# Optimization experiments

Measured on AMD Instinct MI355X. Metric: run time of the kernel, lower is better.

## Reference

```python
import jax, jax.numpy as jnp
import numpy as np

D = 512          # hidden_dim
H_HEADS = 8
DH = D // H_HEADS  # 64
L = 6            # n_layers
P = 8            # patch size
KT = 3           # temporal kernel
Z_DIM = 32
FILM_SCALE = 0.5
ROPE_BASE = 10000.0
EPS = 1e-5


def layer_norm(x, g, b):
    mu = x.mean(-1, keepdims=True)
    var = ((x - mu) ** 2).mean(-1, keepdims=True)
    return (x - mu) * jax.lax.rsqrt(var + EPS) * g + b


def rotate_half(x):
    x1, x2 = jnp.split(x, 2, axis=-1)
    return jnp.concatenate([-x2, x1], axis=-1)


def rope_time(T, dtype):
    half = DH // 2
    inv_freq = ROPE_BASE ** (-(jnp.arange(half, dtype=dtype) / half))  # (half,)
    angles = jnp.arange(T, dtype=dtype)[:, None] * inv_freq[None, :]   # (T, half)
    sin = jnp.concatenate([jnp.sin(angles), jnp.sin(angles)], -1)      # (T, DH)
    cos = jnp.concatenate([jnp.cos(angles), jnp.cos(angles)], -1)
    return sin, cos


def setup_inputs() -> dict:
    key = jax.random.key(0)
    ks = iter(jax.random.split(key, 64))
    n = lambda shape, s=0.02: jax.random.normal(next(ks), shape, jnp.float32) * s
    inp = {
        "x": jax.random.normal(next(ks), (16, 32, 3, 64, 64), jnp.float32),
        "z": jax.random.normal(next(ks), (16, 32, Z_DIM), jnp.float32),
        # tokenizer: CausalConv3d (kt,ph,pw)=(3,8,8), stride (1,8,8)
        "conv_w": n((D, 3, KT, P, P)),
        "conv_b": jnp.zeros((D,), jnp.float32),
        "tok_g": jnp.ones((D,), jnp.float32),
        "tok_b": jnp.zeros((D,), jnp.float32),
        # FiLM from z -> (gamma, beta)
        "film_w": n((Z_DIM, 2 * D)),
        "film_b": jnp.zeros((2 * D,), jnp.float32),
        # transformer blocks (stacked over L)
        "ln1_g": jnp.ones((L, D), jnp.float32), "ln1_b": jnp.zeros((L, D), jnp.float32),
        "kqv_w": n((L, D, 3 * D)), "kqv_b": jnp.zeros((L, 3 * D), jnp.float32),
        "proj_w": n((L, D, D)), "proj_b": jnp.zeros((L, D), jnp.float32),
        "ln2_g": jnp.ones((L, D), jnp.float32), "ln2_b": jnp.zeros((L, D), jnp.float32),
        "mlp_w1": n((L, D, 4 * D)), "mlp_b1": jnp.zeros((L, 4 * D), jnp.float32),
        "mlp_w2": n((L, 4 * D, D)), "mlp_b2": jnp.zeros((L, D), jnp.float32),
        "rs_attn": jnp.full((L,), 0.5, jnp.float32),
        "rs_mlp": jnp.full((L,), 0.5, jnp.float32),
        # scoring head
        "head_g": jnp.ones((D,), jnp.float32), "head_b": jnp.zeros((D,), jnp.float32),
        "head_w": n((D, 1)), "head_bias": jnp.zeros((1,), jnp.float32),
    }
    return inp


def _forward(x, z, conv_w, conv_b, tok_g, tok_b, film_w, film_b,
             ln1_g, ln1_b, kqv_w, kqv_b, proj_w, proj_b, ln2_g, ln2_b,
             mlp_w1, mlp_b1, mlp_w2, mlp_b2, rs_attn, rs_mlp,
             head_g, head_b, head_w, head_bias):
    B, T, C, Himg, Wimg = x.shape
    # ---- SpatialTemporalTokenizer: causal Conv3d (pad time on past only) ----
    xc = jnp.transpose(x, (0, 2, 1, 3, 4))  # [B,C,T,H,W]
    y = jax.lax.conv_general_dilated(
        xc, conv_w, window_strides=(1, P, P),
        padding=[(KT - 1, 0), (0, 0), (0, 0)],
        dimension_numbers=("NCDHW", "OIDHW", "NCDHW"))
    y = y + conv_b[None, :, None, None, None]          # [B,D,T,Hn,Wn]
    Hn, Wn = y.shape[3], y.shape[4]
    tok = jnp.transpose(y, (0, 2, 3, 4, 1)).reshape(B, T, Hn * Wn, D)
    tok = layer_norm(tok, tok_g, tok_b)                 # [B,T,N,D]
    # ---- FiLM conditioning from z ----
    gb = z @ film_w + film_b                            # [B,T,2D]
    gamma, beta = jnp.split(gb, 2, axis=-1)
    tok = (1.0 + FILM_SCALE * gamma)[:, :, None, :] * tok + (FILM_SCALE * beta)[:, :, None, :]
    # ---- spatial pooling -> temporal sequence ----
    h = tok.mean(axis=2)                                # [B,T,D]
    # ---- transformer stack (causal, time RoPE, pre-LN, gated residuals) ----
    sin_t, cos_t = rope_time(T, h.dtype)                # (T, DH)
    causal = jnp.tril(jnp.ones((T, T), bool))
    neg_inf = jnp.finfo(h.dtype).min
    for i in range(L):
        xi = layer_norm(h, ln1_g[i], ln1_b[i])
        kqv = xi @ kqv_w[i] + kqv_b[i]                  # [B,T,3D]
        k, q, v = jnp.split(kqv, 3, axis=-1)            # torch chunk order: k,q,v
        sh = lambda t: t.reshape(B, T, H_HEADS, DH).transpose(0, 2, 1, 3)  # [B,h,T,d]
        q, k, v = sh(q), sh(k), sh(v)
        q = q * cos_t + rotate_half(q) * sin_t
        k = k * cos_t + rotate_half(k) * sin_t
        att = jnp.einsum("bhqd,bhkd->bhqk", q, k) / np.sqrt(DH)
        att = jnp.where(causal[None, None], att, neg_inf)
        att = jax.nn.softmax(att, axis=-1)
        yv = jnp.einsum("bhqk,bhkd->bhqd", att, v)
        yv = yv.transpose(0, 2, 1, 3).reshape(B, T, D)
        attn_out = yv @ proj_w[i] + proj_b[i]
        h = h + rs_attn[i] * attn_out
        x2 = layer_norm(h, ln2_g[i], ln2_b[i])
        m = jax.nn.gelu(x2 @ mlp_w1[i] + mlp_b1[i], approximate=False) @ mlp_w2[i] + mlp_b2[i]
        h = h + rs_mlp[i] * m
    # ---- per-timestep score head ----
    h = layer_norm(h, head_g, head_b)
    score = (h @ head_w + head_bias)[..., 0]            # [B,T]
    return score


def reference(x, z, conv_w, conv_b, tok_g, tok_b, film_w, film_b,
              ln1_g, ln1_b, kqv_w, kqv_b, proj_w, proj_b, ln2_g, ln2_b,
              mlp_w1, mlp_b1, mlp_w2, mlp_b2, rs_attn, rs_mlp,
              head_g, head_b, head_w, head_bias):
    return _forward(x, z, conv_w, conv_b, tok_g, tok_b, film_w, film_b,
                    ln1_g, ln1_b, kqv_w, kqv_b, proj_w, proj_b, ln2_g, ln2_b,
                    mlp_w1, mlp_b1, mlp_w2, mlp_b2, rs_attn, rs_mlp,
                    head_g, head_b, head_w, head_bias)
```

## Files before the change

kernel.cpp:

```cpp
#include <hip/hip_runtime.h>
#include <math.h>

#define EPS 1e-5f

typedef __attribute__((ext_vector_type(8))) short short8;
typedef __attribute__((ext_vector_type(4))) float f32x4;

__device__ __forceinline__ short f2bf(float f) {
    unsigned u = __float_as_uint(f);
    u += 0x7fffu + ((u >> 16) & 1u);
    return (short)(u >> 16);
}
__device__ __forceinline__ float bf2f(short s) {
    return __uint_as_float(((unsigned)(unsigned short)s) << 16);
}
__device__ __forceinline__ void async16(const void* g, void* l) {
    __builtin_amdgcn_global_load_lds(
        (const __attribute__((address_space(1))) unsigned*)g,
        (__attribute__((address_space(3))) unsigned*)l, 16, 0, 0);
}

__device__ __forceinline__ float block_reduce_sum_256(float v, float* red) {
    #pragma unroll
    for (int o = 32; o > 0; o >>= 1) v += __shfl_down(v, o, 64);
    __syncthreads();
    if ((threadIdx.x & 63) == 0) red[threadIdx.x >> 6] = v;
    __syncthreads();
    return red[0] + red[1] + red[2] + red[3];
}

__global__ __launch_bounds__(256) void film_kernel(
    const float* __restrict__ z, const float* __restrict__ fw,
    const float* __restrict__ fb, float* __restrict__ gb) {
    int bt = blockIdx.x;
    __shared__ float zs[32];
    if (threadIdx.x < 32) zs[threadIdx.x] = z[bt * 32 + threadIdx.x];
    __syncthreads();
    for (int j = threadIdx.x; j < 1024; j += 256) {
        float acc = fb[j];
        #pragma unroll
        for (int k = 0; k < 32; k++) acc = fmaf(zs[k], fw[k * 1024 + j], acc);
        gb[bt * 1024 + j] = acc;
    }
}

__global__ __launch_bounds__(256) void cvt_kernel(
    const float* __restrict__ src, short* __restrict__ dst, int n) {
    int i = blockIdx.x * 256 + threadIdx.x;
    if (i < n) dst[i] = f2bf(src[i]);
}

__global__ __launch_bounds__(256) void xcast_kernel(
    const float* __restrict__ x, short* __restrict__ xbf, int n8) {
    int i = blockIdx.x * 256 + threadIdx.x;
    if (i < n8) {
        float4 a = *(const float4*)(x + (size_t)i * 8);
        float4 b = *(const float4*)(x + (size_t)i * 8 + 4);
        short8 o = {f2bf(a.x), f2bf(a.y), f2bf(a.z), f2bf(a.w),
                    f2bf(b.x), f2bf(b.y), f2bf(b.z), f2bf(b.w)};
        *(short8*)(xbf + (size_t)i * 8) = o;
    }
}

__global__ __launch_bounds__(256) void tcast_kernel(
    const float* __restrict__ src, short* __restrict__ dst, int K, int N) {
    __shared__ float tile[32][33];
    src += (size_t)blockIdx.z * K * N;
    dst += (size_t)blockIdx.z * N * K;
    int n0 = blockIdx.x * 32, k0 = blockIdx.y * 32;
    int lx = threadIdx.x & 31, ly = threadIdx.x >> 5;
    #pragma unroll
    for (int i = 0; i < 32; i += 8)
        tile[ly + i][lx] = src[(size_t)(k0 + ly + i) * N + n0 + lx];
    __syncthreads();
    #pragma unroll
    for (int i = 0; i < 32; i += 8)
        dst[(size_t)(n0 + ly + i) * K + k0 + lx] = f2bf(tile[lx][ly + i]);
}

__global__ __launch_bounds__(256) void conv_gemm(
    const short* __restrict__ xbf, const short* __restrict__ wbf,
    const float* __restrict__ cb, short* __restrict__ tok) {
    __shared__ short As[128 * 64];
    __shared__ short Bs[128 * 64];
    int tid = threadIdx.x;
    int n0 = blockIdx.x * 128, m0 = blockIdx.y * 128;
    int wave = tid >> 6, lane = tid & 63, quad = lane >> 4, l16 = lane & 15;
    int wm = wave & 1, wn = wave >> 1;

    int segA[4], tA[4];
    long long base0[4];
    #pragma unroll
    for (int e = 0; e < 4; e++) {
        int p = e * 256 + tid;
        int row = p >> 3;
        segA[e] = (p & 7) ^ (row & 7);
        int m = m0 + row;
        int bt = m >> 6, nn = m & 63;
        int b = bt >> 5, t = bt & 31;
        int hn = nn >> 3, wn2 = nn & 7;
        tA[e] = t;
        base0[e] = (((long long)(b * 32 + t - 2) * 3) << 12)
                   + (long long)(hn * 8) * 64 + wn2 * 8;
    }

    f32x4 acc[4][4];
    #pragma unroll
    for (int mt = 0; mt < 4; mt++)
        #pragma unroll
        for (int nt = 0; nt < 4; nt++) acc[mt][nt] = (f32x4){0.f, 0.f, 0.f, 0.f};

    for (int k0 = 0; k0 < 576; k0 += 64) {
        #pragma unroll
        for (int e = 0; e < 4; e++) {
            int p = e * 256 + tid;
            int n = p >> 3, seg = (p & 7) ^ (n & 7);
            async16(wbf + (size_t)(n0 + n) * 576 + k0 + seg * 8, Bs + p * 8);
        }
        #pragma unroll
        for (int e = 0; e < 4; e++) {
            int p = e * 256 + tid;
            int ks = (k0 >> 3) + segA[e];
            int ch = (ks >= 24) + (ks >= 48);
            int r = ks - ch * 24;
            int kt = r >> 3, ph = r & 7;
            short8 v8 = (short8){0, 0, 0, 0, 0, 0, 0, 0};
            if (tA[e] + kt >= 2)
                v8 = *(const short8*)(xbf + base0[e]
                        + ((long long)(kt * 3 + ch) << 12) + ph * 64);
            *(short8*)(As + p * 8) = v8;
        }
        __syncthreads();
        #pragma unroll
        for (int ksub = 0; ksub < 2; ksub++) {
            int ccb = ksub * 4 + quad;
            short8 af[4], bf[4];
            #pragma unroll
            for (int mt = 0; mt < 4; mt++) {
                int row = wm * 64 + mt * 16 + l16;
                af[mt] = *(const short8*)(As + (row * 8 + (ccb ^ (row & 7))) * 8);
            }
            #pragma unroll
            for (int nt = 0; nt < 4; nt++) {
                int row = wn * 64 + nt * 16 + l16;
                bf[nt] = *(const short8*)(Bs + (row * 8 + (ccb ^ (row & 7))) * 8);
            }
            #pragma unroll
            for (int mt = 0; mt < 4; mt++)
                #pragma unroll
                for (int nt = 0; nt < 4; nt++)
                    acc[mt][nt] = __builtin_amdgcn_mfma_f32_16x16x32_bf16(
                        af[mt], bf[nt], acc[mt][nt], 0, 0, 0);
        }
        __syncthreads();
    }
    #pragma unroll
    for (int mt = 0; mt < 4; mt++)
        #pragma unroll
        for (int nt = 0; nt < 4; nt++)
            #pragma unroll
            for (int reg = 0; reg < 4; reg++) {
                int m = m0 + wm * 64 + mt * 16 + quad * 4 + reg;
                int n = n0 + wn * 64 + nt * 16 + l16;
                tok[(size_t)m * 512 + n] = f2bf(acc[mt][nt][reg] + cb[n]);
            }
}

__global__ __launch_bounds__(256) void tok_post(
    const short* __restrict__ tok, const float* __restrict__ tg,
    const float* __restrict__ tb, const float* __restrict__ gb,
    float* __restrict__ h) {
    __shared__ float mu_s[64], inv_s[64];
    __shared__ float red[4][512];
    int bt = blockIdx.x, tid = threadIdx.x;
    int wave = tid >> 6, lane = tid & 63;
    {
        int tokn = wave * 16 + (lane >> 2), part = lane & 3;
        const short* p = tok + (size_t)(bt * 64 + tokn) * 512 + part * 128;
        float s = 0.f, ss = 0.f;
        #pragma unroll
        for (int i = 0; i < 16; i++) {
            short8 v = *(const short8*)(p + i * 8);
            #pragma unroll
            for (int j = 0; j < 8; j++) {
                float f = bf2f(v[j]);
                s += f; ss += f * f;
            }
        }
        s += __shfl_xor(s, 1, 64); ss += __shfl_xor(ss, 1, 64);
        s += __shfl_xor(s, 2, 64); ss += __shfl_xor(ss, 2, 64);
        if (part == 0) {
            float mu = s * (1.f / 512.f);
            float var = ss * (1.f / 512.f) - mu * mu;
            mu_s[tokn] = mu;
            inv_s[tokn] = rsqrtf(var + EPS);
        }
    }
    __syncthreads();
    float hacc[8] = {0.f, 0.f, 0.f, 0.f, 0.f, 0.f, 0.f, 0.f};
    int c0 = lane * 8;
    for (int it = 0; it < 16; it++) {
        int n = it * 4 + wave;
        float mu = mu_s[n], inv = inv_s[n];
        short8 v = *(const short8*)(tok + (size_t)(bt * 64 + n) * 512 + c0);
        #pragma unroll
        for (int j = 0; j < 8; j++) hacc[j] += (bf2f(v[j]) - mu) * inv;
    }
    #pragma unroll
    for (int j = 0; j < 8; j++) red[wave][c0 + j] = hacc[j];
    __syncthreads();
    #pragma unroll
    for (int cc = 0; cc < 2; cc++) {
        int c = tid + cc * 256;
        float S = red[0][c] + red[1][c] + red[2][c] + red[3][c];
        float G  = 1.f + 0.5f * gb[bt * 1024 + c];
        float Be = 0.5f * gb[bt * 1024 + 512 + c];
        h[bt * 512 + c] = G * (tg[c] * (S * (1.f / 64.f)) + tb[c]) + Be;
    }
}

__global__ __launch_bounds__(256) void gemm_ln(
    const float* __restrict__ hsrc, const float* __restrict__ lng,
    const float* __restrict__ lnb, const short* __restrict__ Bw,
    const float* __restrict__ bias, int N, int mode,
    float* __restrict__ outf, short* __restrict__ outb) {
    __shared__ short As[32 * 512];
    __shared__ short Bs[128 * 128];
    __shared__ float mu_s[32], inv_s[32];
    int tid = threadIdx.x;
    int m0 = blockIdx.y * 32, n0 = blockIdx.x * 128;
    {
        int row = tid >> 3, l8 = tid & 7;
        const float* hp = hsrc + (size_t)(m0 + row) * 512 + l8 * 64;
        float s = 0.f, ss = 0.f;
        #pragma unroll
        for (int i = 0; i < 16; i++) {
            float4 v = *(const float4*)(hp + i * 4);
            s += v.x + v.y + v.z + v.w;
            ss += v.x * v.x + v.y * v.y + v.z * v.z + v.w * v.w;
        }
        s += __shfl_xor(s, 1, 64); ss += __shfl_xor(ss, 1, 64);
        s += __shfl_xor(s, 2, 64); ss += __shfl_xor(ss, 2, 64);
        s += __shfl_xor(s, 4, 64); ss += __shfl_xor(ss, 4, 64);
        if (l8 == 0) {
            float mu = s * (1.f / 512.f);
            float var = ss * (1.f / 512.f) - mu * mu;
            mu_s[row] = mu;
            inv_s[row] = rsqrtf(var + EPS);
        }
    }
    __syncthreads();
    #pragma unroll
    for (int e = 0; e < 8; e++) {
        int lc = e * 256 + tid;
        int row = lc >> 6, cc = lc & 63;
        float mu = mu_s[row], inv = inv_s[row];
        const float* hp = hsrc + (size_t)(m0 + row) * 512 + cc * 8;
        float4 a = *(const float4*)hp, b = *(const float4*)(hp + 4);
        float4 g0 = *(const float4*)(lng + cc * 8), g1 = *(const float4*)(lng + cc * 8 + 4);
        float4 b0 = *(const float4*)(lnb + cc * 8), b1 = *(const float4*)(lnb + cc * 8 + 4);
        short8 o = {f2bf((a.x - mu) * inv * g0.x + b0.x),
                    f2bf((a.y - mu) * inv * g0.y + b0.y),
                    f2bf((a.z - mu) * inv * g0.z + b0.z),
                    f2bf((a.w - mu) * inv * g0.w + b0.w),
                    f2bf((b.x - mu) * inv * g1.x + b1.x),
                    f2bf((b.y - mu) * inv * g1.y + b1.y),
                    f2bf((b.z - mu) * inv * g1.z + b1.z),
                    f2bf((b.w - mu) * inv * g1.w + b1.w)};
        *(short8*)(As + (row * 64 + (cc ^ (row & 7))) * 8) = o;
    }
    __syncthreads();
    int wave = tid >> 6, lane = tid & 63, quad = lane >> 4, l16 = lane & 15;
    f32x4 acc[2][2];
    #pragma unroll
    for (int a2 = 0; a2 < 2; a2++)
        #pragma unroll
        for (int b2 = 0; b2 < 2; b2++) acc[a2][b2] = (f32x4){0.f, 0.f, 0.f, 0.f};
    for (int k0 = 0; k0 < 512; k0 += 128) {
        #pragma unroll
        for (int e = 0; e < 8; e++) {
            int p = e * 256 + tid;
            int row = p >> 4, seg = (p & 15) ^ (row & 15);
            async16(Bw + (size_t)(n0 + row) * 512 + k0 + seg * 8, Bs + p * 8);
        }
        __syncthreads();
        #pragma unroll
        for (int ksub = 0; ksub < 4; ksub++) {
            int ccb = ksub * 4 + quad;
            short8 af[2], bf[2];
            #pragma unroll
            for (int m2 = 0; m2 < 2; m2++) {
                int row = m2 * 16 + l16;
                int cc = (k0 >> 3) + ccb;
                af[m2] = *(const short8*)(As + (row * 64 + (cc ^ (row & 7))) * 8);
            }
            #pragma unroll
            for (int n2 = 0; n2 < 2; n2++) {
                int row = wave * 32 + n2 * 16 + l16;
                bf[n2] = *(const short8*)(Bs + (row * 16 + (ccb ^ (row & 15))) * 8);
            }
            #pragma unroll
            for (int m2 = 0; m2 < 2; m2++)
                #pragma unroll
                for (int n2 = 0; n2 < 2; n2++)
                    acc[m2][n2] = __builtin_amdgcn_mfma_f32_16x16x32_bf16(
                        af[m2], bf[n2], acc[m2][n2], 0, 0, 0);
        }
        __syncthreads();
    }
    #pragma unroll
    for (int m2 = 0; m2 < 2; m2++)
        #pragma unroll
        for (int n2 = 0; n2 < 2; n2++)
            #pragma unroll
            for (int reg = 0; reg < 4; reg++) {
                int m = m0 + m2 * 16 + quad * 4 + reg;
                int n = n0 + wave * 32 + n2 * 16 + l16;
                float v = acc[m2][n2][reg] + bias[n];
                if (mode == 1) {
                    v = 0.5f * v * (1.f + erff(v * 0.70710678118f));
                    outb[(size_t)m * N + n] = f2bf(v);
                } else {
                    outf[(size_t)m * N + n] = v;
                }
            }
}

__global__ __launch_bounds__(256) void gemm_res(
    const short* __restrict__ Ag, const short* __restrict__ Bw,
    const float* __restrict__ bias, const float* __restrict__ rsPtr,
    float* __restrict__ hm, int K) {
    __shared__ short As[32 * 128];
    __shared__ short Bs[64 * 128];
    int tid = threadIdx.x;
    int m0 = blockIdx.y * 32, n0 = blockIdx.x * 64;
    int wave = tid >> 6, lane = tid & 63, quad = lane >> 4, l16 = lane & 15;
    f32x4 acc[2];
    acc[0] = (f32x4){0.f, 0.f, 0.f, 0.f};
    acc[1] = (f32x4){0.f, 0.f, 0.f, 0.f};
    for (int k0 = 0; k0 < K; k0 += 128) {
        #pragma unroll
        for (int e = 0; e < 2; e++) {
            int p = e * 256 + tid;
            int row = p >> 4, seg = (p & 15) ^ (row & 15);
            async16(Ag + (size_t)(m0 + row) * K + k0 + seg * 8, As + p * 8);
        }
        #pragma unroll
        for (int e = 0; e < 4; e++) {
            int p = e * 256 + tid;
            int row = p >> 4, seg = (p & 15) ^ (row & 15);
            async16(Bw + (size_t)(n0 + row) * K + k0 + seg * 8, Bs + p * 8);
        }
        __syncthreads();
        #pragma unroll
        for (int ksub = 0; ksub < 4; ksub++) {
            int ccb = ksub * 4 + quad;
            short8 bf;
            {
                int row = wave * 16 + l16;
                bf = *(const short8*)(Bs + (row * 16 + (ccb ^ (row & 15))) * 8);
            }
            #pragma unroll
            for (int m2 = 0; m2 < 2; m2++) {
                int row = m2 * 16 + l16;
                short8 af = *(const short8*)(As + (row * 16 + (ccb ^ (row & 15))) * 8);
                acc[m2] = __builtin_amdgcn_mfma_f32_16x16x32_bf16(af, bf, acc[m2], 0, 0, 0);
            }
        }
        __syncthreads();
    }
    float rsv = *rsPtr;
    #pragma unroll
    for (int m2 = 0; m2 < 2; m2++)
        #pragma unroll
        for (int reg = 0; reg < 4; reg++) {
            int m = m0 + m2 * 16 + quad * 4 + reg;
            int n = n0 + wave * 16 + l16;
            size_t off = (size_t)m * 512 + n;
            hm[off] = hm[off] + rsv * (acc[m2][reg] + bias[n]);
        }
}

__global__ __launch_bounds__(256) void attn_kernel(
    const float* __restrict__ kqv, short* __restrict__ yv) {
    __shared__ float qs[32][64], ks[32][64], vs[32][64];
    __shared__ float qr[32][64], kr[32][64];
    __shared__ float att[32][32];
    int blk = blockIdx.x;
    int b = blk >> 3, hh = blk & 7;
    int tid = threadIdx.x;

    for (int idx = tid; idx < 2048; idx += 256) {
        int t = idx >> 6, d = idx & 63;
        const float* base = kqv + (size_t)(b * 32 + t) * 1536 + hh * 64 + d;
        ks[t][d] = base[0];
        qs[t][d] = base[512];
        vs[t][d] = base[1024];
    }
    __syncthreads();
    const float lnb = logf(10000.f) / 32.f;
    for (int idx = tid; idx < 2048; idx += 256) {
        int t = idx >> 6, d = idx & 63;
        int j = d & 31;
        float ang = (float)t * expf(-(float)j * lnb);
        float sv = sinf(ang), cv = cosf(ang);
        float qv = qs[t][d], kv = ks[t][d];
        float qo = qs[t][d ^ 32], ko = ks[t][d ^ 32];
        float rq = (d < 32) ? -qo : qo;
        float rk = (d < 32) ? -ko : ko;
        qr[t][d] = qv * cv + rq * sv;
        kr[t][d] = kv * cv + rk * sv;
    }
    __syncthreads();
    #pragma unroll
    for (int l = 0; l < 4; l++) {
        int idx = l * 256 + tid;
        int qt = idx >> 5, kt2 = idx & 31;
        float s;
        if (kt2 > qt) {
            s = -1e30f;
        } else {
            float a = 0.f;
            #pragma unroll
            for (int d = 0; d < 64; d++) a = fmaf(qr[qt][d], kr[kt2][d], a);
            s = a * 0.125f;
        }
        att[qt][kt2] = s;
    }
    __syncthreads();
    if (tid < 32) {
        float m = -1e30f;
        #pragma unroll
        for (int k = 0; k < 32; k++) m = fmaxf(m, att[tid][k]);
        float sum = 0.f;
        #pragma unroll
        for (int k = 0; k < 32; k++) {
            float e = expf(att[tid][k] - m);
            att[tid][k] = e;
            sum += e;
        }
        float inv = 1.f / sum;
        #pragma unroll
        for (int k = 0; k < 32; k++) att[tid][k] *= inv;
    }
    __syncthreads();
    for (int idx = tid; idx < 2048; idx += 256) {
        int t = idx >> 6, d = idx & 63;
        float a = 0.f;
        #pragma unroll
        for (int k = 0; k < 32; k++) a = fmaf(att[t][k], vs[k][d], a);
        yv[(size_t)(b * 32 + t) * 512 + hh * 64 + d] = f2bf(a);
    }
}

__global__ __launch_bounds__(256) void head_kernel(
    const float* __restrict__ h, const float* __restrict__ g,
    const float* __restrict__ bb, const float* __restrict__ w,
    const float* __restrict__ bias0, float* __restrict__ out) {
    __shared__ float red[8];
    int token = blockIdx.x, tid = threadIdx.x;
    float v0 = h[token * 512 + tid], v1 = h[token * 512 + tid + 256];
    float s  = block_reduce_sum_256(v0 + v1, red);
    float ss = block_reduce_sum_256(v0 * v0 + v1 * v1, red);
    float mu = s * (1.f / 512.f);
    float var = ss * (1.f / 512.f) - mu * mu;
    float inv = rsqrtf(var + EPS);
    float n0 = (v0 - mu) * inv * g[tid] + bb[tid];
    float n1 = (v1 - mu) * inv * g[tid + 256] + bb[tid + 256];
    float dot = block_reduce_sum_256(n0 * w[tid] + n1 * w[tid + 256], red);
    if (tid == 0) out[token] = dot + bias0[0];
}

extern "C" void kernel_launch(void* const* d_in, const int* in_sizes, int n_in,
                              void* d_out, int out_size, void* d_ws, size_t ws_size,
                              hipStream_t stream) {
    const float* x       = (const float*)d_in[0];
    const float* z       = (const float*)d_in[1];
    const float* conv_w  = (const float*)d_in[2];
    const float* conv_b  = (const float*)d_in[3];
    const float* tok_g   = (const float*)d_in[4];
    const float* tok_b   = (const float*)d_in[5];
    const float* film_w  = (const float*)d_in[6];
    const float* film_b  = (const float*)d_in[7];
    const float* ln1_g   = (const float*)d_in[8];
    const float* ln1_b   = (const float*)d_in[9];
    const float* kqv_w   = (const float*)d_in[10];
    const float* kqv_b   = (const float*)d_in[11];
    const float* proj_w  = (const float*)d_in[12];
    const float* proj_b  = (const float*)d_in[13];
    const float* ln2_g   = (const float*)d_in[14];
    const float* ln2_b   = (const float*)d_in[15];
    const float* mlp_w1  = (const float*)d_in[16];
    const float* mlp_b1  = (const float*)d_in[17];
    const float* mlp_w2  = (const float*)d_in[18];
    const float* mlp_b2  = (const float*)d_in[19];
    const float* rs_attn = (const float*)d_in[20];
    const float* rs_mlp  = (const float*)d_in[21];
    const float* head_g  = (const float*)d_in[22];
    const float* head_b  = (const float*)d_in[23];
    const float* head_w  = (const float*)d_in[24];
    const float* head_bs = (const float*)d_in[25];
    float* out = (float*)d_out;

    float* ws = (float*)d_ws;
    float* gb   = ws;
    float* h    = gb + 524288;
    float* kqvf = h + 262144;
    short* sb = (short*)(kqvf + 786432);
    short* wbf   = sb;
    short* kqvT  = wbf   + 294912;
    short* projT = kqvT  + 4718592;
    short* mlp1T = projT + 1572864;
    short* mlp2T = mlp1T + 6291456;
    short* tokb  = mlp2T + 6291456;
    short* yvb   = tokb  + 16777216;
    short* mbuf  = yvb   + 262144;
    short* xbf   = mbuf  + 1048576;

    film_kernel<<<512, 256, 0, stream>>>(z, film_w, film_b, gb);
    cvt_kernel<<<1152, 256, 0, stream>>>(conv_w, wbf, 294912);
    xcast_kernel<<<3072, 256, 0, stream>>>(x, xbf, 786432);
    tcast_kernel<<<dim3(48, 16, 6), 256, 0, stream>>>(kqv_w, kqvT, 512, 1536);
    tcast_kernel<<<dim3(16, 16, 6), 256, 0, stream>>>(proj_w, projT, 512, 512);
    tcast_kernel<<<dim3(64, 16, 6), 256, 0, stream>>>(mlp_w1, mlp1T, 512, 2048);
    tcast_kernel<<<dim3(16, 64, 6), 256, 0, stream>>>(mlp_w2, mlp2T, 2048, 512);

    conv_gemm<<<dim3(4, 256), 256, 0, stream>>>(xbf, wbf, conv_b, tokb);
    tok_post<<<512, 256, 0, stream>>>(tokb, tok_g, tok_b, gb, h);

    for (int i = 0; i < 6; i++) {
        gemm_ln<<<dim3(12, 16), 256, 0, stream>>>(
            h, ln1_g + i * 512, ln1_b + i * 512,
            kqvT + (size_t)i * 1536 * 512, kqv_b + i * 1536,
            1536, 0, kqvf, nullptr);
        attn_kernel<<<128, 256, 0, stream>>>(kqvf, yvb);
        gemm_res<<<dim3(8, 16), 256, 0, stream>>>(
            yvb, projT + (size_t)i * 512 * 512, proj_b + i * 512,
            rs_attn + i, h, 512);
        gemm_ln<<<dim3(16, 16), 256, 0, stream>>>(
            h, ln2_g + i * 512, ln2_b + i * 512,
            mlp1T + (size_t)i * 2048 * 512, mlp_b1 + i * 2048,
            2048, 1, nullptr, mbuf);
        gemm_res<<<dim3(8, 16), 256, 0, stream>>>(
            mbuf, mlp2T + (size_t)i * 512 * 2048, mlp_b2 + i * 512,
            rs_mlp + i, h, 2048);
    }

    head_kernel<<<512, 256, 0, stream>>>(h, head_g, head_b, head_w, head_bs, out);
}
```

Baseline: 580.6 us.

## Fuse LN1+QKV GEMM into attention kernel and merge prep kernels

Each block now computes LayerNorm for its batch's 32 tokens, runs the per-head QKV GEMM with MFMA into shared memory, then does RoPE, causal softmax and AV in the same kernel. This removes the fp32 kqv round trip through global memory and one launch per layer. The small preprocessing kernels (film, casts, four transposes) are also merged into two launches. In exchange the QKV GEMM runs on only 128 blocks, each redoing the LayerNorm for its batch row eight times, which lowers parallelism relative to the separate 192-block GEMM.

```diff
diff --git a/kernel.cpp b/kernel.cpp
--- a/kernel.cpp
+++ b/kernel.cpp
@@ -29,31 +29,27 @@
     return red[0] + red[1] + red[2] + red[3];
 }
 
-__global__ __launch_bounds__(256) void film_kernel(
+__global__ __launch_bounds__(256) void prep_misc(
     const float* __restrict__ z, const float* __restrict__ fw,
-    const float* __restrict__ fb, float* __restrict__ gb) {
-    int bt = blockIdx.x;
+    const float* __restrict__ fb, float* __restrict__ gb,
+    const float* __restrict__ conv_w, short* __restrict__ wbf,
+    const float* __restrict__ x, short* __restrict__ xbf) {
     __shared__ float zs[32];
-    if (threadIdx.x < 32) zs[threadIdx.x] = z[bt * 32 + threadIdx.x];
-    __syncthreads();
-    for (int j = threadIdx.x; j < 1024; j += 256) {
-        float acc = fb[j];
-        #pragma unroll
-        for (int k = 0; k < 32; k++) acc = fmaf(zs[k], fw[k * 1024 + j], acc);
-        gb[bt * 1024 + j] = acc;
-    }
-}
-
-__global__ __launch_bounds__(256) void cvt_kernel(
-    const float* __restrict__ src, short* __restrict__ dst, int n) {
-    int i = blockIdx.x * 256 + threadIdx.x;
-    if (i < n) dst[i] = f2bf(src[i]);
-}
-
-__global__ __launch_bounds__(256) void xcast_kernel(
-    const float* __restrict__ x, short* __restrict__ xbf, int n8) {
-    int i = blockIdx.x * 256 + threadIdx.x;
-    if (i < n8) {
+    int bi = blockIdx.x, tid = threadIdx.x;
+    if (bi < 512) {
+        if (tid < 32) zs[tid] = z[bi * 32 + tid];
+        __syncthreads();
+        for (int j = tid; j < 1024; j += 256) {
+            float acc = fb[j];
+            #pragma unroll
+            for (int k = 0; k < 32; k++) acc = fmaf(zs[k], fw[k * 1024 + j], acc);
+            gb[bi * 1024 + j] = acc;
+        }
+    } else if (bi < 1664) {
+        int i = (bi - 512) * 256 + tid;
+        wbf[i] = f2bf(conv_w[i]);
+    } else {
+        int i = (bi - 1664) * 256 + tid;
         float4 a = *(const float4*)(x + (size_t)i * 8);
         float4 b = *(const float4*)(x + (size_t)i * 8 + 4);
         short8 o = {f2bf(a.x), f2bf(a.y), f2bf(a.z), f2bf(a.w),
@@ -62,12 +58,24 @@
     }
 }
 
-__global__ __launch_bounds__(256) void tcast_kernel(
-    const float* __restrict__ src, short* __restrict__ dst, int K, int N) {
+__global__ __launch_bounds__(256) void prep_tcast(
+    const float* __restrict__ kqv_w, short* __restrict__ kqvT,
+    const float* __restrict__ proj_w, short* __restrict__ projT,
+    const float* __restrict__ mlp_w1, short* __restrict__ mlp1T,
+    const float* __restrict__ mlp_w2, short* __restrict__ mlp2T) {
     __shared__ float tile[32][33];
-    src += (size_t)blockIdx.z * K * N;
-    dst += (size_t)blockIdx.z * N * K;
-    int n0 = blockIdx.x * 32, k0 = blockIdx.y * 32;
+    int bi = blockIdx.x;
+    const float* src; short* dst; int NT, K, N, rel;
+    if (bi < 4608)       { src = kqv_w;  dst = kqvT;  NT = 48; K = 512;  N = 1536; rel = bi; }
+    else if (bi < 6144)  { src = proj_w; dst = projT; NT = 16; K = 512;  N = 512;  rel = bi - 4608; }
+    else if (bi < 12288) { src = mlp_w1; dst = mlp1T; NT = 64; K = 512;  N = 2048; rel = bi - 6144; }
+    else                 { src = mlp_w2; dst = mlp2T; NT = 16; K = 2048; N = 512;  rel = bi - 12288; }
+    int per = NT * (K / 32);
+    int layer = rel / per, r2 = rel - layer * per;
+    int nt = r2 % NT, kt = r2 / NT;
+    src += (size_t)layer * K * N;
+    dst += (size_t)layer * N * K;
+    int n0 = nt * 32, k0 = kt * 32;
     int lx = threadIdx.x & 31, ly = threadIdx.x >> 5;
     #pragma unroll
     for (int i = 0; i < 32; i += 8)
@@ -216,6 +224,172 @@
         float G  = 1.f + 0.5f * gb[bt * 1024 + c];
         float Be = 0.5f * gb[bt * 1024 + 512 + c];
         h[bt * 512 + c] = G * (tg[c] * (S * (1.f / 64.f)) + tb[c]) + Be;
+    }
+}
+
+__global__ __launch_bounds__(256) void attn_fused(
+    const float* __restrict__ hsrc, const float* __restrict__ lng,
+    const float* __restrict__ lnb, const short* __restrict__ Bw,
+    const float* __restrict__ bias, short* __restrict__ yv) {
+    __shared__ char smem[57344] __attribute__((aligned(16)));
+    __shared__ float mu_s[32], inv_s[32];
+    short* As = (short*)smem;
+    short* Bs = (short*)(smem + 32768);
+    float (*qs)[64] = (float(*)[64])(smem);
+    float (*ks)[64] = (float(*)[64])(smem + 8192);
+    float (*vs)[64] = (float(*)[64])(smem + 16384);
+    float (*qr)[64] = (float(*)[64])(smem + 24576);
+    float (*kr)[64] = (float(*)[64])(smem + 32768);
+    float (*att)[32] = (float(*)[32])(smem + 40960);
+    int blk = blockIdx.x, b = blk >> 3, hh = blk & 7;
+    int tid = threadIdx.x;
+    int m0 = b * 32;
+    {
+        int row = tid >> 3, l8 = tid & 7;
+        const float* hp = hsrc + (size_t)(m0 + row) * 512 + l8 * 64;
+        float s = 0.f, ss = 0.f;
+        #pragma unroll
+        for (int i = 0; i < 16; i++) {
+            float4 v = *(const float4*)(hp + i * 4);
+            s += v.x + v.y + v.z + v.w;
+            ss += v.x * v.x + v.y * v.y + v.z * v.z + v.w * v.w;
+        }
+        s += __shfl_xor(s, 1, 64); ss += __shfl_xor(ss, 1, 64);
+        s += __shfl_xor(s, 2, 64); ss += __shfl_xor(ss, 2, 64);
+        s += __shfl_xor(s, 4, 64); ss += __shfl_xor(ss, 4, 64);
+        if (l8 == 0) {
+            float mu = s * (1.f / 512.f);
+            float var = ss * (1.f / 512.f) - mu * mu;
+            mu_s[row] = mu;
+            inv_s[row] = rsqrtf(var + EPS);
+        }
+    }
+    __syncthreads();
+    #pragma unroll
+    for (int e = 0; e < 8; e++) {
+        int lc = e * 256 + tid;
+        int row = lc >> 6, cc = lc & 63;
+        float mu = mu_s[row], inv = inv_s[row];
+        const float* hp = hsrc + (size_t)(m0 + row) * 512 + cc * 8;
+        float4 a = *(const float4*)hp, b2 = *(const float4*)(hp + 4);
+        float4 g0 = *(const float4*)(lng + cc * 8), g1 = *(const float4*)(lng + cc * 8 + 4);
+        float4 b0 = *(const float4*)(lnb + cc * 8), b1 = *(const float4*)(lnb + cc * 8 + 4);
+        short8 o = {f2bf((a.x - mu) * inv * g0.x + b0.x),
+                    f2bf((a.y - mu) * inv * g0.y + b0.y),
+                    f2bf((a.z - mu) * inv * g0.z + b0.z),
+                    f2bf((a.w - mu) * inv * g0.w + b0.w),
+                    f2bf((b2.x - mu) * inv * g1.x + b1.x),
+                    f2bf((b2.y - mu) * inv * g1.y + b1.y),
+                    f2bf((b2.z - mu) * inv * g1.z + b1.z),
+                    f2bf((b2.w - mu) * inv * g1.w + b1.w)};
+        *(short8*)(As + (row * 64 + (cc ^ (row & 7))) * 8) = o;
+    }
+    __syncthreads();
+    int wave = tid >> 6, lane = tid & 63, quad = lane >> 4, l16 = lane & 15;
+    f32x4 acc[2][3];
+    #pragma unroll
+    for (int m2 = 0; m2 < 2; m2++)
+        #pragma unroll
+        for (int g = 0; g < 3; g++) acc[m2][g] = (f32x4){0.f, 0.f, 0.f, 0.f};
+    for (int k0 = 0; k0 < 512; k0 += 64) {
+        #pragma unroll
+        for (int e = 0; e < 6; e++) {
+            int p = e * 256 + tid;
+            int row = p >> 3, seg = (p & 7) ^ (row & 7);
+            int n = ((row >> 6) << 9) + hh * 64 + (row & 63);
+            async16(Bw + (size_t)n * 512 + k0 + seg * 8, Bs + p * 8);
+        }
+        __syncthreads();
+        #pragma unroll
+        for (int ksub = 0; ksub < 2; ksub++) {
+            int ccb = ksub * 4 + quad;
+            short8 af[2], bf[3];
+            #pragma unroll
+            for (int m2 = 0; m2 < 2; m2++) {
+                int row = m2 * 16 + l16;
+                int cc = (k0 >> 3) + ccb;
+                af[m2] = *(const short8*)(As + (row * 64 + (cc ^ (row & 7))) * 8);
+            }
+            #pragma unroll
+            for (int g = 0; g < 3; g++) {
+                int row = g * 64 + wave * 16 + l16;
+                bf[g] = *(const short8*)(Bs + (row * 8 + (ccb ^ (row & 7))) * 8);
+            }
+            #pragma unroll
+            for (int m2 = 0; m2 < 2; m2++)
+                #pragma unroll
+                for (int g = 0; g < 3; g++)
+                    acc[m2][g] = __builtin_amdgcn_mfma_f32_16x16x32_bf16(
+                        af[m2], bf[g], acc[m2][g], 0, 0, 0);
+        }
+        __syncthreads();
+    }
+    float bb0 = bias[hh * 64 + wave * 16 + l16];
+    float bb1 = bias[512 + hh * 64 + wave * 16 + l16];
+    float bb2 = bias[1024 + hh * 64 + wave * 16 + l16];
+    int dcol = wave * 16 + l16;
+    #pragma unroll
+    for (int m2 = 0; m2 < 2; m2++)
+        #pragma unroll
+        for (int reg = 0; reg < 4; reg++) {
+            int tkn = m2 * 16 + quad * 4 + reg;
+            ks[tkn][dcol] = acc[m2][0][reg] + bb0;
+            qs[tkn][dcol] = acc[m2][1][reg] + bb1;
+            vs[tkn][dcol] = acc[m2][2][reg] + bb2;
+        }
+    __syncthreads();
+    const float lnb_c = logf(10000.f) / 32.f;
+    for (int idx = tid; idx < 2048; idx += 256) {
+        int t = idx >> 6, d = idx & 63;
+        int j = d & 31;
+        float ang = (float)t * expf(-(float)j * lnb_c);
+        float sv = sinf(ang), cv = cosf(ang);
+        float qv = qs[t][d], kv = ks[t][d];
+        float qo = qs[t][d ^ 32], ko = ks[t][d ^ 32];
+        float rq = (d < 32) ? -qo : qo;
+        float rk = (d < 32) ? -ko : ko;
+        qr[t][d] = qv * cv + rq * sv;
+        kr[t][d] = kv * cv + rk * sv;
+    }
+    __syncthreads();
+    #pragma unroll
+    for (int l = 0; l < 4; l++) {
+        int idx = l * 256 + tid;
+        int qt = idx >> 5, kt2 = idx & 31;
+        float s;
+        if (kt2 > qt) {
+            s = -1e30f;
+        } else {
+            float a = 0.f;
+            #pragma unroll
+            for (int d = 0; d < 64; d++) a = fmaf(qr[qt][d], kr[kt2][d], a);
+            s = a * 0.125f;
+        }
+        att[qt][kt2] = s;
+    }
+    __syncthreads();
+    if (tid < 32) {
+        float m = -1e30f;
+        #pragma unroll
+        for (int k = 0; k < 32; k++) m = fmaxf(m, att[tid][k]);
+        float sum = 0.f;
+        #pragma unroll
+        for (int k = 0; k < 32; k++) {
+            float e = expf(att[tid][k] - m);
+            att[tid][k] = e;
+            sum += e;
+        }
+        float inv = 1.f / sum;
+        #pragma unroll
+        for (int k = 0; k < 32; k++) att[tid][k] *= inv;
+    }
+    __syncthreads();
+    for (int idx = tid; idx < 2048; idx += 256) {
+        int t = idx >> 6, d = idx & 63;
+        float a = 0.f;
+        #pragma unroll
+        for (int k = 0; k < 32; k++) a = fmaf(att[t][k], vs[k][d], a);
+        yv[(size_t)(b * 32 + t) * 512 + hh * 64 + d] = f2bf(a);
     }
 }
 
@@ -379,78 +553,6 @@
             size_t off = (size_t)m * 512 + n;
             hm[off] = hm[off] + rsv * (acc[m2][reg] + bias[n]);
         }
-}
-
-__global__ __launch_bounds__(256) void attn_kernel(
-    const float* __restrict__ kqv, short* __restrict__ yv) {
-    __shared__ float qs[32][64], ks[32][64], vs[32][64];
-    __shared__ float qr[32][64], kr[32][64];
-    __shared__ float att[32][32];
-    int blk = blockIdx.x;
-    int b = blk >> 3, hh = blk & 7;
-    int tid = threadIdx.x;
-
-    for (int idx = tid; idx < 2048; idx += 256) {
-        int t = idx >> 6, d = idx & 63;
-        const float* base = kqv + (size_t)(b * 32 + t) * 1536 + hh * 64 + d;
-        ks[t][d] = base[0];
-        qs[t][d] = base[512];
-        vs[t][d] = base[1024];
-    }
-    __syncthreads();
-    const float lnb = logf(10000.f) / 32.f;
-    for (int idx = tid; idx < 2048; idx += 256) {
-        int t = idx >> 6, d = idx & 63;
-        int j = d & 31;
-        float ang = (float)t * expf(-(float)j * lnb);
-        float sv = sinf(ang), cv = cosf(ang);
-        float qv = qs[t][d], kv = ks[t][d];
-        float qo = qs[t][d ^ 32], ko = ks[t][d ^ 32];
-        float rq = (d < 32) ? -qo : qo;
-        float rk = (d < 32) ? -ko : ko;
-        qr[t][d] = qv * cv + rq * sv;
-        kr[t][d] = kv * cv + rk * sv;
-    }
-    __syncthreads();
-    #pragma unroll
-    for (int l = 0; l < 4; l++) {
-        int idx = l * 256 + tid;
-        int qt = idx >> 5, kt2 = idx & 31;
-        float s;
-        if (kt2 > qt) {
-            s = -1e30f;
-        } else {
-            float a = 0.f;
-            #pragma unroll
-            for (int d = 0; d < 64; d++) a = fmaf(qr[qt][d], kr[kt2][d], a);
-            s = a * 0.125f;
-        }
-        att[qt][kt2] = s;
-    }
-    __syncthreads();
-    if (tid < 32) {
-        float m = -1e30f;
-        #pragma unroll
-        for (int k = 0; k < 32; k++) m = fmaxf(m, att[tid][k]);
-        float sum = 0.f;
-        #pragma unroll
-        for (int k = 0; k < 32; k++) {
-            float e = expf(att[tid][k] - m);
-            att[tid][k] = e;
-            sum += e;
-        }
-        float inv = 1.f / sum;
-        #pragma unroll
-        for (int k = 0; k < 32; k++) att[tid][k] *= inv;
-    }
-    __syncthreads();
-    for (int idx = tid; idx < 2048; idx += 256) {
-        int t = idx >> 6, d = idx & 63;
-        float a = 0.f;
-        #pragma unroll
-        for (int k = 0; k < 32; k++) a = fmaf(att[t][k], vs[k][d], a);
-        yv[(size_t)(b * 32 + t) * 512 + hh * 64 + d] = f2bf(a);
-    }
 }
 
 __global__ __launch_bounds__(256) void head_kernel(
@@ -505,8 +607,7 @@
     float* ws = (float*)d_ws;
     float* gb   = ws;
     float* h    = gb + 524288;
-    float* kqvf = h + 262144;
-    short* sb = (short*)(kqvf + 786432);
+    short* sb = (short*)(h + 262144);
     short* wbf   = sb;
     short* kqvT  = wbf   + 294912;
     short* projT = kqvT  + 4718592;
@@ -517,23 +618,17 @@
     short* mbuf  = yvb   + 262144;
     short* xbf   = mbuf  + 1048576;
 
-    film_kernel<<<512, 256, 0, stream>>>(z, film_w, film_b, gb);
-    cvt_kernel<<<1152, 256, 0, stream>>>(conv_w, wbf, 294912);
-    xcast_kernel<<<3072, 256, 0, stream>>>(x, xbf, 786432);
-    tcast_kernel<<<dim3(48, 16, 6), 256, 0, stream>>>(kqv_w, kqvT, 512, 1536);
-    tcast_kernel<<<dim3(16, 16, 6), 256, 0, stream>>>(proj_w, projT, 512, 512);
-    tcast_kernel<<<dim3(64, 16, 6), 256, 0, stream>>>(mlp_w1, mlp1T, 512, 2048);
-    tcast_kernel<<<dim3(16, 64, 6), 256, 0, stream>>>(mlp_w2, mlp2T, 2048, 512);
+    prep_misc<<<4736, 256, 0, stream>>>(z, film_w, film_b, gb, conv_w, wbf, x, xbf);
+    prep_tcast<<<18432, 256, 0, stream>>>(kqv_w, kqvT, proj_w, projT,
+                                          mlp_w1, mlp1T, mlp_w2, mlp2T);
 
     conv_gemm<<<dim3(4, 256), 256, 0, stream>>>(xbf, wbf, conv_b, tokb);
     tok_post<<<512, 256, 0, stream>>>(tokb, tok_g, tok_b, gb, h);
 
     for (int i = 0; i < 6; i++) {
-        gemm_ln<<<dim3(12, 16), 256, 0, stream>>>(
+        attn_fused<<<128, 256, 0, stream>>>(
             h, ln1_g + i * 512, ln1_b + i * 512,
-            kqvT + (size_t)i * 1536 * 512, kqv_b + i * 1536,
-            1536, 0, kqvf, nullptr);
-        attn_kernel<<<128, 256, 0, stream>>>(kqvf, yvb);
+            kqvT + (size_t)i * 1536 * 512, kqv_b + i * 1536, yvb);
         gemm_res<<<dim3(8, 16), 256, 0, stream>>>(
             yvb, projT + (size_t)i * 512 * 512, proj_b + i * 512,
             rs_attn + i, h, 512);
```

New measurement: 549.8 us. -5.3%, faster.
